# Kernel optimization log

Hardware: AMD Instinct MI355X
Metric: run time of the kernel (lower is better)

## Reference

```python
import jax, jax.numpy as jnp
import numpy as np

PERCENTAGE = 0.26
BN_EPS = 1e-5


def _conv1x1(x, w, b):
    # x: (B,C,H,W), w: (O,C), b: (O,)
    return jnp.einsum('bchw,oc->bohw', x, w) + b[None, :, None, None]


def _bn_train(x, gamma, beta):
    # BatchNorm2d in training mode: biased variance over (B,H,W) per channel
    mean = x.mean(axis=(0, 2, 3), keepdims=True)
    var = jnp.mean((x - mean) ** 2, axis=(0, 2, 3), keepdims=True)
    xhat = (x - mean) * jax.lax.rsqrt(var + BN_EPS)
    return xhat * gamma[None, :, None, None] + beta[None, :, None, None]


def _band_mask(w, max_w):
    # The two mask-construction loops in the torch code reduce to |i-j| < max_w
    idx = jnp.arange(w)
    return jnp.abs(idx[:, None] - idx[None, :]) < max_w  # (w, w) bool


def setup_inputs() -> dict:
    key = jax.random.key(0)
    ks = jax.random.split(key, 16)
    B, C, H, W = 2, 256, 64, 512
    s = 0.02  # weight scale to keep attention logits in a sane range
    return {
        'x1': jax.random.normal(ks[0], (B, C, H, W), jnp.float32),
        'x2': jax.random.normal(ks[1], (B, C, H, W), jnp.float32),
        'Qw': jax.random.normal(ks[2], (C, C), jnp.float32) * s,
        'Qb': jax.random.normal(ks[3], (C,), jnp.float32) * s,
        'Kw': jax.random.normal(ks[4], (C, C), jnp.float32) * s,
        'Kb': jax.random.normal(ks[5], (C,), jnp.float32) * s,
        'Vw': jax.random.normal(ks[6], (C, C), jnp.float32) * s,
        'Vb': jax.random.normal(ks[7], (C,), jnp.float32) * s,
        'Vg': jax.random.normal(ks[8], (C,), jnp.float32),
        'Vbeta': jax.random.normal(ks[9], (C,), jnp.float32),
        'Ww': jax.random.normal(ks[10], (C, C), jnp.float32) * s,
        'Wb': jax.random.normal(ks[11], (C,), jnp.float32) * s,
        'Wg': jax.random.normal(ks[12], (C,), jnp.float32),
        'Wbeta': jax.random.normal(ks[13], (C,), jnp.float32),
    }


def reference(x1, x2, Qw, Qb, Kw, Kb, Vw, Vb, Vg, Vbeta, Ww, Wb, Wg, Wbeta):
    b, c, h, w = x1.shape
    max_w = int(w * PERCENTAGE)
    mask = _band_mask(w, max_w)  # (w, w), broadcasts over (b*h) rows
    neg_inf = jnp.float32(-jnp.inf)

    def rows(x):  # (B,C,H,W) -> (B*H, W, C)
        return x.transpose(0, 2, 3, 1).reshape(b * h, w, c)

    q1 = rows(_conv1x1(x1, Qw, Qb))
    q2 = rows(_conv1x1(x2, Qw, Qb))
    k1 = rows(_conv1x1(x1, Kw, Kb))  # (B*H, W, C); contract over C below
    k2 = rows(_conv1x1(x2, Kw, Kb))
    v1 = rows(_bn_train(_conv1x1(x1, Vw, Vb), Vg, Vbeta))
    v2 = rows(_bn_train(_conv1x1(x2, Vw, Vb), Vg, Vbeta))

    def attend(q, k, v):
        scores = jnp.einsum('nqc,nkc->nqk', q, k)  # (B*H, W, W)
        scores = jnp.where(mask[None], scores, neg_inf)
        p = jax.nn.softmax(scores, axis=-1)
        return jnp.einsum('nqk,nkc->nqc', p, v)

    def cols(y):  # (B*H, W, C) -> (B,C,H,W)
        return y.reshape(b, h, w, c).transpose(0, 3, 1, 2)

    y1 = cols(attend(q1, k2, v2))
    y2 = cols(attend(q2, k1, v1))
    z1 = _bn_train(_conv1x1(y1, Ww, Wb), Wg, Wbeta) + x1
    z2 = _bn_train(_conv1x1(y2, Ww, Wb), Wg, Wbeta) + x2
    return (z1, z2)
```

## Files before the change

### kernel.cpp

```cpp
#include <hip/hip_runtime.h>

typedef unsigned short u16;
typedef short bfrag __attribute__((ext_vector_type(8)));
typedef float ffrag __attribute__((ext_vector_type(4)));
typedef u16 u16x4 __attribute__((ext_vector_type(4)));

#define MFMA16(a,b,c) __builtin_amdgcn_mfma_f32_16x16x32_bf16((a),(b),(c),0,0,0)

#define WAITV(N) do { asm volatile("s_waitcnt vmcnt(" #N ")" ::: "memory"); \
                      __builtin_amdgcn_sched_barrier(0); } while(0)
#define RBAR()   do { __builtin_amdgcn_s_barrier(); \
                      __builtin_amdgcn_sched_barrier(0); } while(0)


__device__ __forceinline__ u16 f2bf(float f){
  union { float f; unsigned int i; } cv; cv.f = f;
  unsigned int x = cv.i;
  return (u16)((x + 0x7fffu + ((x >> 16) & 1u)) >> 16);
}
__device__ __forceinline__ float bf2f(u16 u){
  union { unsigned int i; float f; } cv;
  cv.i = ((unsigned int)u) << 16;
  return cv.f;
}
__device__ __forceinline__ bfrag ldb(const u16* p){
  bfrag v; __builtin_memcpy(&v, p, 16); return v;
}
__device__ __forceinline__ void gload_lds16(const u16* g, u16* l){
  __builtin_amdgcn_global_load_lds(
      (const __attribute__((address_space(1))) unsigned int*)g,
      (__attribute__((address_space(3))) unsigned int*)l, 16, 0, 0);
}

__global__ __launch_bounds__(256) void k_wcvt(const float* __restrict__ qw, const float* __restrict__ kw,
                                              const float* __restrict__ vw, const float* __restrict__ ww,
                                              u16* __restrict__ out){
  int t = blockIdx.x*256 + threadIdx.x;
  out[t]        = f2bf(qw[t]);
  out[t+65536]  = f2bf(kw[t]);
  out[t+131072] = f2bf(vw[t]);
  out[t+196608] = f2bf(ww[t]);
}

__global__ __launch_bounds__(256) void k_xpose(const float* __restrict__ x1, const float* __restrict__ x2,
                                               u16* __restrict__ xr1, u16* __restrict__ xr2){
  const float* x = blockIdx.z ? x2 : x1;
  u16* xr = blockIdx.z ? xr2 : xr1;
  __shared__ float T[64][65];
  int t = threadIdx.x;
  int p0 = blockIdx.x*64, c0 = blockIdx.y*64;
  int b = p0 >> 15, q0 = p0 & 32767;
  #pragma unroll
  for (int it=0; it<4; ++it){
    int cc = it*16 + (t>>4);
    int pi = (t&15)*4;
    ffrag v; __builtin_memcpy(&v, x + ((size_t)(b*256 + c0 + cc))*32768 + q0 + pi, 16);
    T[cc][pi+0]=v[0]; T[cc][pi+1]=v[1]; T[cc][pi+2]=v[2]; T[cc][pi+3]=v[3];
  }
  __syncthreads();
  int pi = t>>2, cj0 = (t&3)*16;
  u16 tmp[16];
  #pragma unroll
  for (int j=0;j<16;++j) tmp[j] = f2bf(T[cj0+j][pi]);
  __builtin_memcpy(xr + (size_t)(p0+pi)*256 + c0 + cj0, tmp, 32);
}

__device__ __forceinline__ void stage_tile(const u16* __restrict__ src, int row0, int k0,
                                           u16* lds, int wid, int l){
  #pragma unroll
  for (int rr=0; rr<4; ++rr){
    int off = rr*4096 + wid*1024 + l*16;
    int row = off>>7, inb = off&127;
    int srcb = inb ^ ((row&7)<<4);
    gload_lds16(src + (size_t)(row0+row)*256 + k0 + (srcb>>1),
                lds + ((rr*4096 + wid*1024)>>1));
  }
}

__global__ __launch_bounds__(256, 2) void k_qkv(const u16* __restrict__ xr1, const u16* __restrict__ xr2,
    const u16* __restrict__ wb,
    const float* __restrict__ qb, const float* __restrict__ kb, const float* __restrict__ vb,
    u16* __restrict__ Q1, u16* __restrict__ K1, u16* __restrict__ V1,
    u16* __restrict__ Q2, u16* __restrict__ K2, u16* __restrict__ V2){
  __shared__ __align__(16) u16 As[2][8192];
  __shared__ __align__(16) u16 Bs[2][8192];
  int id = blockIdx.x;
  int xcd = id & 7, j = id >> 3;
  int pl = j/12, v = j - pl*12;
  int ptile = xcd*64 + pl;
  int ot = v & 1, r = v >> 1;
  int wgt = r >> 1, s = r & 1;
  const u16* A = s ? xr2 : xr1;
  const u16* W = wb + wgt*65536;
  const float* bias = (wgt==0)? qb : (wgt==1)? kb : vb;

  int t = threadIdx.x, wid = t>>6, l = t&63, lr = l&15, lg = l>>4;
  int p0 = ptile*128, o0 = ot*128;
  int wr = (wid>>1)*64, wc = (wid&1)*64;
  int swz = (lr&7)<<4;

  stage_tile(A, p0, 0, As[0], wid, l);
  stage_tile(W, o0, 0, Bs[0], wid, l);

  const ffrag fz = {0.f,0.f,0.f,0.f};
  ffrag acc[4][4];
  #pragma unroll
  for (int i=0;i<4;++i){ acc[i][0]=fz; acc[i][1]=fz; acc[i][2]=fz; acc[i][3]=fz; }

  #pragma unroll
  for (int ks=0; ks<4; ++ks){
    __syncthreads();
    if (ks < 3){
      stage_tile(A, p0, (ks+1)*64, As[(ks+1)&1], wid, l);
      stage_tile(W, o0, (ks+1)*64, Bs[(ks+1)&1], wid, l);
    }
    const u16* as = As[ks&1];
    const u16* bs = Bs[ks&1];
    #pragma unroll
    for (int kc=0; kc<2; ++kc){
      int colb = (kc*64 + lg*16) ^ swz;
      bfrag af[4], bfm[4];
      #pragma unroll
      for (int mt=0; mt<4; ++mt)
        af[mt] = ldb(as + (((wr + mt*16 + lr)*128 + colb)>>1));
      #pragma unroll
      for (int nt=0; nt<4; ++nt)
        bfm[nt] = ldb(bs + (((wc + nt*16 + lr)*128 + colb)>>1));
      #pragma unroll
      for (int mt=0; mt<4; ++mt)
        #pragma unroll
        for (int nt=0; nt<4; ++nt)
          acc[mt][nt] = MFMA16(af[mt], bfm[nt], acc[mt][nt]);
    }
  }

  u16* Qo = s ? Q2 : Q1;
  u16* Ko = s ? K2 : K1;
  u16* Vt = s ? V2 : V1;
  #pragma unroll
  for (int nt=0; nt<4; ++nt){
    int oo = o0 + wc + nt*16 + lr;
    float bsc = bias[oo];
    #pragma unroll
    for (int mt=0; mt<4; ++mt){
      int pr = p0 + wr + mt*16 + lg*4;
      if (wgt == 2){
        int n = pr >> 9, w0 = pr & 511;
        u16x4 vv;
        #pragma unroll
        for (int rr=0;rr<4;++rr) vv[rr] = f2bf(acc[mt][nt][rr] + bsc);
        *reinterpret_cast<u16x4*>(Vt + ((size_t)(n*256 + oo))*512 + w0) = vv;
      } else {
        u16* op = (wgt==0)? Qo : Ko;
        #pragma unroll
        for (int rr=0;rr<4;++rr)
          op[(size_t)(pr + rr)*256 + oo] = f2bf(acc[mt][nt][rr] + bsc);
      }
    }
  }
}

__global__ __launch_bounds__(256, 2) void k_conv1(const u16* __restrict__ in1, const u16* __restrict__ in2,
    const u16* __restrict__ wp, const float* __restrict__ bias,
    u16* __restrict__ o1, u16* __restrict__ o2,
    float* __restrict__ psum, float* __restrict__ psq){
  __shared__ __align__(16) u16 As[2][8192];
  __shared__ __align__(16) u16 Bs[2][8192];
  int id = blockIdx.x;
  int xcd = id & 7, j = id >> 3;
  int pl = j>>2, v = j&3;
  int ptile = xcd*64 + pl;
  int ot = v & 1, s = v >> 1;
  const u16* A = s ? in2 : in1;
  u16* out = s ? o2 : o1;

  int t = threadIdx.x, wid = t>>6, l = t&63, lr = l&15, lg = l>>4;
  int p0 = ptile*128, o0 = ot*128;
  int wr = (wid>>1)*64, wc = (wid&1)*64;
  int swz = (lr&7)<<4;

  stage_tile(A, p0, 0, As[0], wid, l);
  stage_tile(wp, o0, 0, Bs[0], wid, l);

  const ffrag fz = {0.f,0.f,0.f,0.f};
  ffrag acc[4][4];
  #pragma unroll
  for (int i=0;i<4;++i){ acc[i][0]=fz; acc[i][1]=fz; acc[i][2]=fz; acc[i][3]=fz; }

  #pragma unroll
  for (int ks=0; ks<4; ++ks){
    __syncthreads();
    if (ks < 3){
      stage_tile(A, p0, (ks+1)*64, As[(ks+1)&1], wid, l);
      stage_tile(wp, o0, (ks+1)*64, Bs[(ks+1)&1], wid, l);
    }
    const u16* as = As[ks&1];
    const u16* bs = Bs[ks&1];
    #pragma unroll
    for (int kc=0; kc<2; ++kc){
      int colb = (kc*64 + lg*16) ^ swz;
      bfrag af[4], bfm[4];
      #pragma unroll
      for (int mt=0; mt<4; ++mt)
        af[mt] = ldb(as + (((wr + mt*16 + lr)*128 + colb)>>1));
      #pragma unroll
      for (int nt=0; nt<4; ++nt)
        bfm[nt] = ldb(bs + (((wc + nt*16 + lr)*128 + colb)>>1));
      #pragma unroll
      for (int mt=0; mt<4; ++mt)
        #pragma unroll
        for (int nt=0; nt<4; ++nt)
          acc[mt][nt] = MFMA16(af[mt], bfm[nt], acc[mt][nt]);
    }
  }

  float pv[4], qv[4];
  #pragma unroll
  for (int nt=0; nt<4; ++nt){ pv[nt]=0.f; qv[nt]=0.f; }
  #pragma unroll
  for (int nt=0; nt<4; ++nt){
    int oo = o0 + wc + nt*16 + lr;
    float bsc = bias[oo];
    #pragma unroll
    for (int mt=0; mt<4; ++mt){
      int pr = p0 + wr + mt*16 + lg*4;
      #pragma unroll
      for (int rr=0;rr<4;++rr){
        float val = acc[mt][nt][rr] + bsc;
        out[(size_t)(pr + rr)*256 + oo] = f2bf(val);
        pv[nt] += val; qv[nt] += val*val;
      }
    }
  }
  #pragma unroll
  for (int nt=0; nt<4; ++nt){
    float sv = pv[nt], sq = qv[nt];
    sv += __shfl_xor(sv,16,64); sv += __shfl_xor(sv,32,64);
    sq += __shfl_xor(sq,16,64); sq += __shfl_xor(sq,32,64);
    if (lg==0){
      int oo = o0 + wc + nt*16 + lr;
      int idx = ((s*256 + oo)<<10) + (ptile<<1) + (wr>>6);
      psum[idx] = sv; psq[idx] = sq;
    }
  }
}

__global__ __launch_bounds__(256) void k_vstat1(const u16* __restrict__ V1, const u16* __restrict__ V2,
                                                float* __restrict__ ps, float* __restrict__ pq){
  int s = blockIdx.z;
  const u16* Vt = s ? V2 : V1;
  int c = blockIdx.x, ch = blockIdx.y, t = threadIdx.x;
  float sm=0.f, sq=0.f;
  for (int nn=0; nn<16; ++nn){
    const u16* row = Vt + ((size_t)((ch*16+nn)*256 + c))*512 + t;
    float v = bf2f(row[0]);   sm+=v; sq+=v*v;
    v = bf2f(row[256]);       sm+=v; sq+=v*v;
  }
  __shared__ float rs[256], rq[256];
  rs[t]=sm; rq[t]=sq; __syncthreads();
  for (int st=128; st>0; st>>=1){ if (t<st){ rs[t]+=rs[t+st]; rq[t]+=rq[t+st]; } __syncthreads(); }
  if (t==0){ ps[s*2048 + c*8+ch]=rs[0]; pq[s*2048 + c*8+ch]=rq[0]; }
}
__global__ __launch_bounds__(256) void k_vstat2(const float* __restrict__ ps, const float* __restrict__ pq,
                                                const float* __restrict__ g, const float* __restrict__ be,
                                                float* __restrict__ aVall, float* __restrict__ bVall){
  int s = blockIdx.x, c = threadIdx.x;
  float sm=0.f, sq=0.f;
  #pragma unroll
  for (int ch=0; ch<8; ++ch){ sm += ps[s*2048 + c*8+ch]; sq += pq[s*2048 + c*8+ch]; }
  float mean = sm*(1.f/65536.f);
  float var  = sq*(1.f/65536.f) - mean*mean;
  float aa = g[c]*rsqrtf(var + 1e-5f);
  aVall[s*256+c]=aa; bVall[s*256+c]=be[c]-aa*mean;
}

__device__ __forceinline__ void stageK(const u16* Kn, u16* kb, int kt, int wid, int l){
  #pragma unroll
  for (int c2=0; c2<2; ++c2){
    int off = wid*2048 + c2*1024 + l*16;
    int row = off>>9, inb = off&511;
    int src = inb ^ ((row&7)<<4);
    gload_lds16(Kn + (size_t)(kt*16+row)*256 + (src>>1), kb + wid*1024 + c2*512);
  }
}
__device__ __forceinline__ void stageV(const u16* Vn, u16* vb, int k0, int wid, int l){
  #pragma unroll
  for (int c4=0; c4<4; ++c4){
    int off = wid*4096 + c4*1024 + l*16;
    int crow = off>>6, slot = (off>>4)&3;
    int kk = slot ^ ((crow>>1)&3);
    gload_lds16(Vn + (size_t)crow*512 + k0 + (kk<<3), vb + ((wid*4096 + c4*1024)>>1));
  }
}

__global__ __launch_bounds__(256) void k_attn(
    const u16* __restrict__ Q1, const u16* __restrict__ K2, const u16* __restrict__ V2,
    const u16* __restrict__ Q2, const u16* __restrict__ K1, const u16* __restrict__ V1,
    const float* __restrict__ aVall, const float* __restrict__ bVall,
    u16* __restrict__ O1, u16* __restrict__ O2){
  __shared__ __align__(16) u16 SB[24576];
  int t = threadIdx.x, wid = t>>6, l = t&63, lr = l&15, lg = l>>4;
  int id = blockIdx.x;
  int s = id >> 10;
  int r0 = id & 1023;
  int xcd = r0 & 7, s5 = r0 >> 3;
  int qb = s5 & 7, n = (xcd<<4) | (s5>>3);
  const u16* Q = s ? Q2 : Q1;
  const u16* K = s ? K1 : K2;
  const u16* V = s ? V1 : V2;
  const float* aV = aVall + (s ? 0 : 256);
  const float* bV = bVall + (s ? 0 : 256);
  u16* O = s ? O2 : O1;

  int q0 = qb*64, q0w = q0 + wid*16;
  int lo = q0 - 132; if (lo < 0) lo = 0;
  int hi = q0 + 195; if (hi > 511) hi = 511;
  int KTLO = (lo>>4) & ~1;
  int KTHI = (hi>>4) | 1;
  int NT = KTHI - KTLO + 1;
  int NK1 = NT - 1;
  int nksp = NT >> 1;

  const u16* Kn = K + (size_t)n*131072;
  const u16* Vn = V + (size_t)n*131072;

  bfrag qa[8];
  const u16* Qrow = Q + ((size_t)(n*512 + q0w + lr))*256 + lg*8;
  #pragma unroll
  for (int ks=0; ks<8; ++ks) qa[ks] = ldb(Qrow + ks*32);
  WAITV(0);

  stageK(Kn, SB + 0*4096, KTLO+0, wid, l);
  stageK(Kn, SB + 1*4096, KTLO+1, wid, l);
  stageK(Kn, SB + 2*4096, KTLO+2, wid, l);

  const ffrag fz = {0.f,0.f,0.f,0.f};
  ffrag acc[24];
  #pragma unroll
  for (int i=0;i<24;++i) acc[i] = fz;

  #pragma unroll
  for (int j=0; j<24; ++j){
    if (j < NT){
      WAITV(4); RBAR();
      int jn = j+3; if (jn > NK1) jn = NK1;
      stageK(Kn, SB + ((j+3)&3)*4096, KTLO+jn, wid, l);
      const u16* kbuf = SB + (j&3)*4096;
      #pragma unroll
      for (int ks=0; ks<8; ++ks){
        int boff = (ks*64 + lg*16) ^ ((lr&7)<<4);
        bfrag kf = ldb(kbuf + lr*256 + (boff>>1));
        acc[j] = MFMA16(kf, qa[ks], acc[j]);
      }
    }
  }
  WAITV(0); RBAR();

  stageV(Vn, SB + 0*8192, KTLO*16 + 0*32, wid, l);
  stageV(Vn, SB + 1*8192, KTLO*16 + 1*32, wid, l);

  int q = q0w + lr;
  float m = -1e30f;
  #pragma unroll
  for (int j=0;j<24;++j){
    if (j < NT){
      int colb = (KTLO+j)*16 + lg*4;
      #pragma unroll
      for (int r=0;r<4;++r){
        int d = q - (colb + r);
        bool v = (d < 133) && (d > -133);
        m = v ? fmaxf(m, acc[j][r]) : m;
      }
    }
  }
  m = fmaxf(m, __shfl_xor(m, 16, 64));
  m = fmaxf(m, __shfl_xor(m, 32, 64));
  float sum = 0.f;
  #pragma unroll
  for (int j=0;j<24;++j){
    if (j < NT){
      int colb = (KTLO+j)*16 + lg*4;
      #pragma unroll
      for (int r=0;r<4;++r){
        int d = q - (colb + r);
        bool v = (d < 133) && (d > -133);
        float e = v ? __expf(acc[j][r] - m) : 0.f;
        acc[j][r] = e; sum += e;
      }
    }
  }
  sum += __shfl_xor(sum, 16, 64);
  sum += __shfl_xor(sum, 32, 64);
  float rinv = 1.f / sum;

  unsigned pk0[24], pk1[24];
  #pragma unroll
  for (int j=0;j<24;++j){
    if (j < NT){
      pk0[j] = (unsigned)f2bf(acc[j][0]*rinv) | ((unsigned)f2bf(acc[j][1]*rinv) << 16);
      pk1[j] = (unsigned)f2bf(acc[j][2]*rinv) | ((unsigned)f2bf(acc[j][3]*rinv) << 16);
    } else { pk0[j] = 0u; pk1[j] = 0u; }
  }

  int s0l = lr + (lg&1)*32;
  bool hi2 = (lg & 2) != 0;
  int vswz = (lg ^ ((lr>>1)&3))<<3;
  ffrag o[16];
  #pragma unroll
  for (int i=0;i<16;++i) o[i] = fz;

  #pragma unroll
  for (int ksp=0; ksp<12; ++ksp){
    if (ksp < nksp){
      WAITV(4); RBAR();
      int kn = ksp+2; if (kn > nksp-1) kn = nksp-1;
      stageV(Vn, SB + ((ksp+2)%3)*8192, KTLO*16 + kn*32, wid, l);

      unsigned a0 = (unsigned)__shfl((int)pk0[2*ksp],   s0l,    64);
      unsigned a1 = (unsigned)__shfl((int)pk1[2*ksp],   s0l,    64);
      unsigned a2 = (unsigned)__shfl((int)pk0[2*ksp],   s0l+16, 64);
      unsigned a3 = (unsigned)__shfl((int)pk1[2*ksp],   s0l+16, 64);
      unsigned b0 = (unsigned)__shfl((int)pk0[2*ksp+1], s0l,    64);
      unsigned b1 = (unsigned)__shfl((int)pk1[2*ksp+1], s0l,    64);
      unsigned b2 = (unsigned)__shfl((int)pk0[2*ksp+1], s0l+16, 64);
      unsigned b3 = (unsigned)__shfl((int)pk1[2*ksp+1], s0l+16, 64);
      unsigned pu[4];
      pu[0] = hi2 ? b0 : a0;  pu[1] = hi2 ? b1 : a1;
      pu[2] = hi2 ? b2 : a2;  pu[3] = hi2 ? b3 : a3;
      bfrag pa; __builtin_memcpy(&pa, pu, 16);

      const u16* vbuf = SB + (ksp%3)*8192;
      #pragma unroll
      for (int ct=0; ct<16; ++ct){
        bfrag vf = ldb(vbuf + (ct*16 + lr)*32 + vswz);
        o[ct] = MFMA16(pa, vf, o[ct]);
      }
    }
  }

  #pragma unroll
  for (int ct=0; ct<16; ++ct){
    int c = ct*16 + lr;
    float av = aV[c], bv = bV[c];
    #pragma unroll
    for (int r=0;r<4;++r)
      O[((size_t)(n*512 + q0w + lg*4 + r))*256 + c] = f2bf(av*o[ct][r] + bv);
  }
}

__global__ __launch_bounds__(256) void k_ustat2(const float* __restrict__ psum, const float* __restrict__ psq,
                                                const float* __restrict__ g, const float* __restrict__ be,
                                                float* __restrict__ aWall, float* __restrict__ bWall){
  int c = blockIdx.x, s = blockIdx.y, t = threadIdx.x;
  const float* ps = psum + (((size_t)s*256 + c)<<10);
  const float* pq = psq  + (((size_t)s*256 + c)<<10);
  float sm = ps[t] + ps[t+256] + ps[t+512] + ps[t+768];
  float sq = pq[t] + pq[t+256] + pq[t+512] + pq[t+768];
  __shared__ float rs[256], rq[256];
  rs[t]=sm; rq[t]=sq; __syncthreads();
  for (int st=128; st>0; st>>=1){ if (t<st){ rs[t]+=rs[t+st]; rq[t]+=rq[t+st]; } __syncthreads(); }
  if (t==0){
    float mean = rs[0]*(1.f/65536.f);
    float var  = rq[0]*(1.f/65536.f) - mean*mean;
    float aa = g[c]*rsqrtf(var + 1e-5f);
    aWall[s*256+c]=aa; bWall[s*256+c]=be[c]-aa*mean;
  }
}

__global__ __launch_bounds__(256) void k_final(const u16* __restrict__ u1, const u16* __restrict__ u2,
                                               const u16* __restrict__ xr1, const u16* __restrict__ xr2,
                                               const float* __restrict__ aWall, const float* __restrict__ bWall,
                                               float* __restrict__ z){
  int s = blockIdx.z;
  const u16* u  = s ? u2 : u1;
  const u16* xr = s ? xr2 : xr1;
  const float* aW = aWall + s*256;
  const float* bW = bWall + s*256;
  float* zb = z + (size_t)s*16777216;
  __shared__ u16 Tu[64][66], Tx[64][66];
  int t = threadIdx.x;
  int p0 = blockIdx.x*64, c0 = blockIdx.y*64;
  int b = p0>>15, q0 = p0&32767;
  #pragma unroll
  for (int it=0; it<4; ++it){
    int pi = it*16 + (t>>4);
    int cj = (t&15)*4;
    u16x4 vu; __builtin_memcpy(&vu, u  + (size_t)(p0+pi)*256 + c0 + cj, 8);
    u16x4 vx; __builtin_memcpy(&vx, xr + (size_t)(p0+pi)*256 + c0 + cj, 8);
    *reinterpret_cast<u16x4*>(&Tu[pi][cj]) = vu;
    *reinterpret_cast<u16x4*>(&Tx[pi][cj]) = vx;
  }
  __syncthreads();
  #pragma unroll
  for (int it=0; it<16; ++it){
    int cc = it*4 + (t>>6);
    int qi = t&63;
    size_t addr = ((size_t)(b*256 + c0 + cc))*32768 + q0 + qi;
    zb[addr] = aW[c0+cc]*bf2f(Tu[qi][cc]) + bW[c0+cc] + bf2f(Tx[qi][cc]);
  }
}

extern "C" void kernel_launch(void* const* d_in, const int* in_sizes, int n_in,
                              void* d_out, int out_size, void* d_ws, size_t ws_size,
                              hipStream_t stream) {
  const float* x1  = (const float*)d_in[0];
  const float* x2  = (const float*)d_in[1];
  const float* Qw  = (const float*)d_in[2];
  const float* Qb  = (const float*)d_in[3];
  const float* Kw  = (const float*)d_in[4];
  const float* Kb  = (const float*)d_in[5];
  const float* Vw  = (const float*)d_in[6];
  const float* Vb  = (const float*)d_in[7];
  const float* Vg  = (const float*)d_in[8];
  const float* Vbe = (const float*)d_in[9];
  const float* Ww  = (const float*)d_in[10];
  const float* Wb  = (const float*)d_in[11];
  const float* Wg  = (const float*)d_in[12];
  const float* Wbe = (const float*)d_in[13];

  char* ws = (char*)d_ws;
  const size_t S = 33554432;
  u16* xr1 = (u16*)(ws + 0*S);
  u16* xr2 = (u16*)(ws + 1*S);
  u16* Q1  = (u16*)(ws + 2*S);
  u16* K1  = (u16*)(ws + 3*S);
  u16* Q2  = (u16*)(ws + 4*S);
  u16* K2  = (u16*)(ws + 5*S);
  u16* wb  = (u16*)(ws + 6*S);
  float* vec = (float*)(ws + 6*S + 524288);
  float* aVall = vec;
  float* bVall = vec + 512;
  float* aWall = vec + 1024;
  float* bWall = vec + 1536;
  float* vps   = vec + 2048;
  float* vpq   = vps + 4096;

  char* douts = (char*)d_out;
  u16* Vt1 = (u16*)douts;
  u16* Vt2 = (u16*)(douts + S);
  u16* O1  = (u16*)(douts + 2*S);
  u16* O2  = (u16*)(douts + 3*S);
  float* upsum = (float*)douts;
  float* upsq  = upsum + 524288;
  u16* u1 = Q1;  u16* u2 = K1;
  float* z = (float*)d_out;

  dim3 gt(1024, 4, 2);
  dim3 gv(256, 8, 2);
  dim3 gu2(256, 2);

  k_wcvt<<<256, 256, 0, stream>>>(Qw, Kw, Vw, Ww, wb);
  k_xpose<<<gt, 256, 0, stream>>>(x1, x2, xr1, xr2);
  k_qkv<<<6144, 256, 0, stream>>>(xr1, xr2, wb, Qb, Kb, Vb, Q1, K1, Vt1, Q2, K2, Vt2);
  k_vstat1<<<gv, 256, 0, stream>>>(Vt1, Vt2, vps, vpq);
  k_vstat2<<<2, 256, 0, stream>>>(vps, vpq, Vg, Vbe, aVall, bVall);
  k_attn<<<2048, 256, 0, stream>>>(Q1, K2, Vt2, Q2, K1, Vt1, aVall, bVall, O1, O2);
  k_conv1<<<2048, 256, 0, stream>>>(O1, O2, wb + 196608, Wb, u1, u2, upsum, upsq);
  k_ustat2<<<gu2, 256, 0, stream>>>(upsum, upsq, Wg, Wbe, aWall, bWall);
  k_final<<<gt, 256, 0, stream>>>(u1, u2, xr1, xr2, aWall, bWall, z);
}
```

Baseline: 386.2 us.

## Fuse attention QK and PV into online-softmax loop; deepen GEMM prefetch

The attention kernel goes from two passes (compute all banded scores, then softmax, then stream V) to a single flash-style loop. Each step loads two K tiles and one V tile into double buffers, keeps a running max and sum, and rescales the output lazily only when the max grows by more than a threshold. The projection GEMMs now prefetch two K-chunks ahead with explicit vmcnt waits instead of one ahead. This removes the serial split between the K and V streaming phases and cuts register pressure from holding all scores. In exchange it adds per-step reductions, shuffles and an extra barrier.

New measurement: 415.7 us. 7.6% more time.

```diff
diff --git a/kernel.cpp b/kernel.cpp
--- a/kernel.cpp
+++ b/kernel.cpp
@@ -99,8 +99,10 @@
   int wr = (wid>>1)*64, wc = (wid&1)*64;
   int swz = (lr&7)<<4;
 
-  stage_tile(A, p0, 0, As[0], wid, l);
-  stage_tile(W, o0, 0, Bs[0], wid, l);
+  stage_tile(A, p0, 0,  As[0], wid, l);
+  stage_tile(W, o0, 0,  Bs[0], wid, l);
+  stage_tile(A, p0, 64, As[1], wid, l);
+  stage_tile(W, o0, 64, Bs[1], wid, l);
 
   const ffrag fz = {0.f,0.f,0.f,0.f};
   ffrag acc[4][4];
@@ -109,11 +111,8 @@
 
   #pragma unroll
   for (int ks=0; ks<4; ++ks){
-    __syncthreads();
-    if (ks < 3){
-      stage_tile(A, p0, (ks+1)*64, As[(ks+1)&1], wid, l);
-      stage_tile(W, o0, (ks+1)*64, Bs[(ks+1)&1], wid, l);
-    }
+    if (ks < 3) { WAITV(8); } else { WAITV(0); }
+    RBAR();
     const u16* as = As[ks&1];
     const u16* bs = Bs[ks&1];
     #pragma unroll
@@ -131,6 +130,11 @@
         #pragma unroll
         for (int nt=0; nt<4; ++nt)
           acc[mt][nt] = MFMA16(af[mt], bfm[nt], acc[mt][nt]);
+    }
+    RBAR();
+    if (ks < 2){
+      stage_tile(A, p0, (ks+2)*64, As[ks&1], wid, l);
+      stage_tile(W, o0, (ks+2)*64, Bs[ks&1], wid, l);
     }
   }
 
@@ -179,8 +183,10 @@
   int wr = (wid>>1)*64, wc = (wid&1)*64;
   int swz = (lr&7)<<4;
 
-  stage_tile(A, p0, 0, As[0], wid, l);
+  stage_tile(A, p0, 0,  As[0], wid, l);
   stage_tile(wp, o0, 0, Bs[0], wid, l);
+  stage_tile(A, p0, 64, As[1], wid, l);
+  stage_tile(wp, o0, 64,Bs[1], wid, l);
 
   const ffrag fz = {0.f,0.f,0.f,0.f};
   ffrag acc[4][4];
@@ -189,11 +195,8 @@
 
   #pragma unroll
   for (int ks=0; ks<4; ++ks){
-    __syncthreads();
-    if (ks < 3){
-      stage_tile(A, p0, (ks+1)*64, As[(ks+1)&1], wid, l);
-      stage_tile(wp, o0, (ks+1)*64, Bs[(ks+1)&1], wid, l);
-    }
+    if (ks < 3) { WAITV(8); } else { WAITV(0); }
+    RBAR();
     const u16* as = As[ks&1];
     const u16* bs = Bs[ks&1];
     #pragma unroll
@@ -211,6 +214,11 @@
         #pragma unroll
         for (int nt=0; nt<4; ++nt)
           acc[mt][nt] = MFMA16(af[mt], bfm[nt], acc[mt][nt]);
+    }
+    RBAR();
+    if (ks < 2){
+      stage_tile(A, p0, (ks+2)*64, As[ks&1], wid, l);
+      stage_tile(wp, o0, (ks+2)*64, Bs[ks&1], wid, l);
     }
   }
 
@@ -298,7 +306,8 @@
     const u16* __restrict__ Q2, const u16* __restrict__ K1, const u16* __restrict__ V1,
     const float* __restrict__ aVall, const float* __restrict__ bVall,
     u16* __restrict__ O1, u16* __restrict__ O2){
-  __shared__ __align__(16) u16 SB[24576];
+  __shared__ __align__(16) u16 KP[2][8192];
+  __shared__ __align__(16) u16 VBs[2][8192];
   int t = threadIdx.x, wid = t>>6, l = t&63, lr = l&15, lg = l>>4;
   int id = blockIdx.x;
   int s = id >> 10;
@@ -317,9 +326,7 @@
   int hi = q0 + 195; if (hi > 511) hi = 511;
   int KTLO = (lo>>4) & ~1;
   int KTHI = (hi>>4) | 1;
-  int NT = KTHI - KTLO + 1;
-  int NK1 = NT - 1;
-  int nksp = NT >> 1;
+  int nsteps = (KTHI - KTLO + 2) >> 1;
 
   const u16* Kn = K + (size_t)n*131072;
   const u16* Vn = V + (size_t)n*131072;
@@ -330,121 +337,121 @@
   for (int ks=0; ks<8; ++ks) qa[ks] = ldb(Qrow + ks*32);
   WAITV(0);
 
-  stageK(Kn, SB + 0*4096, KTLO+0, wid, l);
-  stageK(Kn, SB + 1*4096, KTLO+1, wid, l);
-  stageK(Kn, SB + 2*4096, KTLO+2, wid, l);
+  stageK(Kn, KP[0],        KTLO+0, wid, l);
+  stageK(Kn, KP[0]+4096,   KTLO+1, wid, l);
+  stageV(Vn, VBs[0],       KTLO*16 + 0,  wid, l);
+  stageK(Kn, KP[1],        KTLO+2, wid, l);
+  stageK(Kn, KP[1]+4096,   KTLO+3, wid, l);
+  stageV(Vn, VBs[1],       KTLO*16 + 32, wid, l);
 
   const ffrag fz = {0.f,0.f,0.f,0.f};
-  ffrag acc[24];
-  #pragma unroll
-  for (int i=0;i<24;++i) acc[i] = fz;
-
-  #pragma unroll
-  for (int j=0; j<24; ++j){
-    if (j < NT){
-      WAITV(4); RBAR();
-      int jn = j+3; if (jn > NK1) jn = NK1;
-      stageK(Kn, SB + ((j+3)&3)*4096, KTLO+jn, wid, l);
-      const u16* kbuf = SB + (j&3)*4096;
-      #pragma unroll
-      for (int ks=0; ks<8; ++ks){
-        int boff = (ks*64 + lg*16) ^ ((lr&7)<<4);
-        bfrag kf = ldb(kbuf + lr*256 + (boff>>1));
-        acc[j] = MFMA16(kf, qa[ks], acc[j]);
-      }
-    }
-  }
-  WAITV(0); RBAR();
-
-  stageV(Vn, SB + 0*8192, KTLO*16 + 0*32, wid, l);
-  stageV(Vn, SB + 1*8192, KTLO*16 + 1*32, wid, l);
-
+  ffrag o[16];
+  #pragma unroll
+  for (int i=0;i<16;++i) o[i] = fz;
+  float m_run = -1e30f, lsum = 0.f;
   int q = q0w + lr;
-  float m = -1e30f;
-  #pragma unroll
-  for (int j=0;j<24;++j){
-    if (j < NT){
-      int colb = (KTLO+j)*16 + lg*4;
-      #pragma unroll
-      for (int r=0;r<4;++r){
-        int d = q - (colb + r);
-        bool v = (d < 133) && (d > -133);
-        m = v ? fmaxf(m, acc[j][r]) : m;
-      }
-    }
-  }
-  m = fmaxf(m, __shfl_xor(m, 16, 64));
-  m = fmaxf(m, __shfl_xor(m, 32, 64));
-  float sum = 0.f;
-  #pragma unroll
-  for (int j=0;j<24;++j){
-    if (j < NT){
-      int colb = (KTLO+j)*16 + lg*4;
-      #pragma unroll
-      for (int r=0;r<4;++r){
-        int d = q - (colb + r);
-        bool v = (d < 133) && (d > -133);
-        float e = v ? __expf(acc[j][r] - m) : 0.f;
-        acc[j][r] = e; sum += e;
-      }
-    }
-  }
-  sum += __shfl_xor(sum, 16, 64);
-  sum += __shfl_xor(sum, 32, 64);
-  float rinv = 1.f / sum;
-
-  unsigned pk0[24], pk1[24];
-  #pragma unroll
-  for (int j=0;j<24;++j){
-    if (j < NT){
-      pk0[j] = (unsigned)f2bf(acc[j][0]*rinv) | ((unsigned)f2bf(acc[j][1]*rinv) << 16);
-      pk1[j] = (unsigned)f2bf(acc[j][2]*rinv) | ((unsigned)f2bf(acc[j][3]*rinv) << 16);
-    } else { pk0[j] = 0u; pk1[j] = 0u; }
-  }
-
   int s0l = lr + (lg&1)*32;
   bool hi2 = (lg & 2) != 0;
   int vswz = (lg ^ ((lr>>1)&3))<<3;
-  ffrag o[16];
-  #pragma unroll
-  for (int i=0;i<16;++i) o[i] = fz;
-
-  #pragma unroll
-  for (int ksp=0; ksp<12; ++ksp){
-    if (ksp < nksp){
-      WAITV(4); RBAR();
-      int kn = ksp+2; if (kn > nksp-1) kn = nksp-1;
-      stageV(Vn, SB + ((ksp+2)%3)*8192, KTLO*16 + kn*32, wid, l);
-
-      unsigned a0 = (unsigned)__shfl((int)pk0[2*ksp],   s0l,    64);
-      unsigned a1 = (unsigned)__shfl((int)pk1[2*ksp],   s0l,    64);
-      unsigned a2 = (unsigned)__shfl((int)pk0[2*ksp],   s0l+16, 64);
-      unsigned a3 = (unsigned)__shfl((int)pk1[2*ksp],   s0l+16, 64);
-      unsigned b0 = (unsigned)__shfl((int)pk0[2*ksp+1], s0l,    64);
-      unsigned b1 = (unsigned)__shfl((int)pk1[2*ksp+1], s0l,    64);
-      unsigned b2 = (unsigned)__shfl((int)pk0[2*ksp+1], s0l+16, 64);
-      unsigned b3 = (unsigned)__shfl((int)pk1[2*ksp+1], s0l+16, 64);
+
+  #pragma unroll
+  for (int sp=0; sp<12; ++sp){
+    if (sp < nsteps){
+      if (sp < nsteps-1) { WAITV(8); } else { WAITV(0); }
+      RBAR();
+      const u16* kp = KP[sp&1];
+      const u16* vb = VBs[sp&1];
+
+      ffrag sA = fz, sB = fz;
+      #pragma unroll
+      for (int ks=0; ks<8; ++ks){
+        int boff = (ks*64 + lg*16) ^ ((lr&7)<<4);
+        bfrag kfA = ldb(kp + ((lr*512 + boff)>>1));
+        bfrag kfB = ldb(kp + 4096 + ((lr*512 + boff)>>1));
+        sA = MFMA16(kfA, qa[ks], sA);
+        sB = MFMA16(kfB, qa[ks], sB);
+      }
+
+      int colbA = (KTLO + 2*sp)*16 + lg*4;
+      bool vA[4], vB[4];
+      float mt = -1e30f;
+      #pragma unroll
+      for (int r=0;r<4;++r){
+        int dA = q - (colbA + r);
+        int dB = dA - 16;
+        vA[r] = (dA < 133) && (dA > -133);
+        vB[r] = (dB < 133) && (dB > -133);
+        mt = vA[r] ? fmaxf(mt, sA[r]) : mt;
+        mt = vB[r] ? fmaxf(mt, sB[r]) : mt;
+      }
+      mt = fmaxf(mt, __shfl_xor(mt, 16, 64));
+      mt = fmaxf(mt, __shfl_xor(mt, 32, 64));
+      if (!__all(mt <= m_run + 8.f)){
+        float mn = fmaxf(m_run, mt);
+        float sc = __expf(m_run - mn);
+        float scr0 = __shfl(sc, (lg<<2)+0, 64);
+        float scr1 = __shfl(sc, (lg<<2)+1, 64);
+        float scr2 = __shfl(sc, (lg<<2)+2, 64);
+        float scr3 = __shfl(sc, (lg<<2)+3, 64);
+        #pragma unroll
+        for (int ct=0; ct<16; ++ct){
+          o[ct][0]*=scr0; o[ct][1]*=scr1; o[ct][2]*=scr2; o[ct][3]*=scr3;
+        }
+        lsum *= sc; m_run = mn;
+      }
+      float es = 0.f;
+      #pragma unroll
+      for (int r=0;r<4;++r){
+        float eA = vA[r] ? __expf(sA[r] - m_run) : 0.f;
+        float eB = vB[r] ? __expf(sB[r] - m_run) : 0.f;
+        sA[r] = eA; sB[r] = eB; es += eA + eB;
+      }
+      es += __shfl_xor(es, 16, 64);
+      es += __shfl_xor(es, 32, 64);
+      lsum += es;
+
+      unsigned pk0A = (unsigned)f2bf(sA[0]) | ((unsigned)f2bf(sA[1])<<16);
+      unsigned pk1A = (unsigned)f2bf(sA[2]) | ((unsigned)f2bf(sA[3])<<16);
+      unsigned pk0B = (unsigned)f2bf(sB[0]) | ((unsigned)f2bf(sB[1])<<16);
+      unsigned pk1B = (unsigned)f2bf(sB[2]) | ((unsigned)f2bf(sB[3])<<16);
+      unsigned a0 = (unsigned)__shfl((int)pk0A, s0l,    64);
+      unsigned a1 = (unsigned)__shfl((int)pk1A, s0l,    64);
+      unsigned a2 = (unsigned)__shfl((int)pk0A, s0l+16, 64);
+      unsigned a3 = (unsigned)__shfl((int)pk1A, s0l+16, 64);
+      unsigned b0 = (unsigned)__shfl((int)pk0B, s0l,    64);
+      unsigned b1 = (unsigned)__shfl((int)pk1B, s0l,    64);
+      unsigned b2 = (unsigned)__shfl((int)pk0B, s0l+16, 64);
+      unsigned b3 = (unsigned)__shfl((int)pk1B, s0l+16, 64);
       unsigned pu[4];
       pu[0] = hi2 ? b0 : a0;  pu[1] = hi2 ? b1 : a1;
       pu[2] = hi2 ? b2 : a2;  pu[3] = hi2 ? b3 : a3;
       bfrag pa; __builtin_memcpy(&pa, pu, 16);
 
-      const u16* vbuf = SB + (ksp%3)*8192;
       #pragma unroll
       for (int ct=0; ct<16; ++ct){
-        bfrag vf = ldb(vbuf + (ct*16 + lr)*32 + vswz);
+        bfrag vf = ldb(vb + (ct*16 + lr)*32 + vswz);
         o[ct] = MFMA16(pa, vf, o[ct]);
       }
-    }
-  }
-
+      RBAR();
+      if (sp+2 < nsteps){
+        stageK(Kn, KP[sp&1],      KTLO + 2*sp + 4, wid, l);
+        stageK(Kn, KP[sp&1]+4096, KTLO + 2*sp + 5, wid, l);
+        stageV(Vn, VBs[sp&1],     KTLO*16 + (sp+2)*32, wid, l);
+      }
+    }
+  }
+
+  float rinv = 1.f / lsum;
+  float linv[4];
+  #pragma unroll
+  for (int r=0;r<4;++r) linv[r] = __shfl(rinv, (lg<<2)+r, 64);
   #pragma unroll
   for (int ct=0; ct<16; ++ct){
     int c = ct*16 + lr;
     float av = aV[c], bv = bV[c];
     #pragma unroll
     for (int r=0;r<4;++r)
-      O[((size_t)(n*512 + q0w + lg*4 + r))*256 + c] = f2bf(av*o[ct][r] + bv);
+      O[((size_t)(n*512 + q0w + lg*4 + r))*256 + c] = f2bf(av*(o[ct][r]*linv[r]) + bv);
   }
 }
 
```
